# Performance work log

Measured on AMD Instinct MI355X. Metric: run time of the kernel, lower is better.

## Reference

```python
import jax, jax.numpy as jnp
import numpy as np
from jax import lax

B, L, C, H, W = 16, 8, 64, 50, 50
OC, K, PAD = 64, 3, 1
CQ = C // 16


def conv2d(x, w, b, pad):
    y = lax.conv_general_dilated(x, w, (1, 1), [(pad, pad), (pad, pad)],
                                 dimension_numbers=('NCHW', 'OIHW', 'NCHW'))
    return y + b[None, :, None, None]


def attention(x, y, q_w, q_b, k_w, k_b, v_w, v_b):
    # x, y: [b, C, 5, 5]
    b, c, h, w = x.shape
    q = conv2d(x, q_w, q_b, 1).reshape(b, -1, h * w)   # [b, CQ, N]
    kk = conv2d(y, k_w, k_b, 1).reshape(b, -1, h * w)  # [b, CQ, N]
    attn = jax.nn.softmax(jnp.einsum('bcn,bcm->bnm', q, kk), axis=-1)  # [b, Nq, Nk]
    v = conv2d(y, v_w, v_b, 1).reshape(b, c, h * w)    # [b, C, N]
    out = jnp.einsum('bcm,bnm->bcn', v, attn)          # bmm(V, attn^T)
    return out.reshape(b, c, h, w)


def setup_inputs():
    key = jax.random.key(0)
    ks = jax.random.split(key, 15)
    s = 0.05
    return {
        'x': jax.random.normal(ks[0], (B, L, C, H, W), jnp.float32),
        'weight': jax.random.normal(ks[1], (OC, C, K, K), jnp.float32) * s,
        'bias': jax.random.normal(ks[2], (OC,), jnp.float32) * s,
        'init_w': jax.random.normal(ks[3], (C, C, 3, 3), jnp.float32) * s,
        'init_b': jax.random.normal(ks[4], (C,), jnp.float32) * s,
        'q_w': jax.random.normal(ks[5], (CQ, C, 3, 3), jnp.float32) * s,
        'q_b': jax.random.normal(ks[6], (CQ,), jnp.float32) * s,
        'k_w': jax.random.normal(ks[7], (CQ, C, 3, 3), jnp.float32) * s,
        'k_b': jax.random.normal(ks[8], (CQ,), jnp.float32) * s,
        'v_w': jax.random.normal(ks[9], (C, C, 3, 3), jnp.float32) * s,
        'v_b': jax.random.normal(ks[10], (C,), jnp.float32) * s,
        'tconv_w': jax.random.normal(ks[11], (C, C), jnp.float32) * s,  # 1x1x1 Conv3d C->C
        'tconv_b': jax.random.normal(ks[12], (C,), jnp.float32) * s,
        'fc_w': jax.random.normal(ks[13], (C,), jnp.float32) * s,       # 1x1x1 Conv3d C->1
        'fc_b': jax.random.normal(ks[14], (), jnp.float32) * s,
    }


def reference(x, weight, bias, init_w, init_b, q_w, q_b, k_w, k_b, v_w, v_b,
              tconv_w, tconv_b, fc_w, fc_b):
    b, l, c, h, w = x.shape
    # --- generateweight ---
    xet = jnp.transpose(x, (0, 2, 1, 3, 4))  # [b, c, l, h, w]
    # AdaptiveMaxPool3d((None,5,5)); h,w multiples of 5 -> exact reshape max
    pooled = xet.reshape(b, c, l, 5, h // 5, 5, w // 5).max((4, 6))  # [b,c,l,5,5]
    seq = jnp.moveaxis(pooled, 2, 0)  # [l, b, c, 5, 5]
    prior0 = conv2d(seq[0], init_w, init_b, 1)

    def step(prior, xt):
        new = attention(prior, xt, q_w, q_b, k_w, k_b, v_w, v_b)
        return new, new

    _, allp = lax.scan(step, prior0, seq)            # [l, b, c, 5, 5]
    avg = jnp.moveaxis(allp, 0, 2).mean((3, 4))      # AdaptiveAvgPool3d -> [b, c, l]
    calib = jnp.einsum('oc,bcl->bol', tconv_w, avg) + tconv_b[None, :, None]  # [b,c,l]
    scale = 1.0 + jnp.transpose(calib, (0, 2, 1))    # [b, l, c]
    # finalweight[b,l,o,i,kh,kw] = weight[o,i,kh,kw] * scale[b,l,i]
    fw = weight[None, None] * scale[:, :, None, :, None, None]
    fc_out = jnp.einsum('c,bcl->bl', fc_w, avg) + fc_b  # [b, l]
    fb = bias[None, None, :] * (1.0 + fc_out)[:, :, None]  # [b, l, oc]
    # --- grouped conv with groups = b*l ---
    xg = x.reshape(1, b * l * c, h, w)
    wg = fw.reshape(b * l * OC, c, K, K)
    out = lax.conv_general_dilated(xg, wg, (1, 1), [(PAD, PAD), (PAD, PAD)],
                                   feature_group_count=b * l,
                                   dimension_numbers=('NCHW', 'OIHW', 'NCHW'))
    out = out.reshape(b * l, OC, out.shape[-2], out.shape[-1])
    out = out + fb.reshape(b * l, OC)[:, :, None, None]
    return out
```

## Files before the change

kernel.cpp:

```cpp
#include <hip/hip_runtime.h>

typedef short s16x8 __attribute__((ext_vector_type(8)));
typedef float f32x4 __attribute__((ext_vector_type(4)));

__device__ __forceinline__ unsigned short bf16r(float f) {
  unsigned int u = __float_as_uint(f);
  u += 0x7fffu + ((u >> 16) & 1u);
  return (unsigned short)(u >> 16);
}


__global__ __launch_bounds__(256) void poolprep2_kernel(
    const float* __restrict__ x, float* __restrict__ pooled,
    unsigned short* __restrict__ xs) {
  const int blk = blockIdx.x;
  const int g = blk / 10;
  const int rem = blk % 10;
  const int band = rem >> 1;
  const int chalf = rem & 1;
  const int ch0 = chalf * 4;
  const float* xg = x + (size_t)g * 160000;
  unsigned short* xsg = xs + (size_t)g * (52 * 52 * 64);
  __shared__ float pm2[32 * 250];
  const int tid = threadIdx.x;

  for (int task = tid; task < 1000; task += 256) {
    int chunk4 = task & 3;
    int rest = task >> 2;
    int xpair = rest % 25;
    int r = rest / 25;
    int y = band * 10 + r;
    int chunk = ch0 + chunk4;
    const float* base = xg + (chunk * 8) * 2500 + y * 50 + xpair * 2;
    float2 v[8];
#pragma unroll
    for (int k = 0; k < 8; ++k) v[k] = *(const float2*)(base + k * 2500);
#pragma unroll
    for (int k = 0; k < 8; ++k)
      pm2[(chunk4 * 8 + k) * 250 + r * 25 + xpair] = fmaxf(v[k].x, v[k].y);
    uint4 a, b;
    a.x = (unsigned)bf16r(v[0].x) | ((unsigned)bf16r(v[1].x) << 16);
    a.y = (unsigned)bf16r(v[2].x) | ((unsigned)bf16r(v[3].x) << 16);
    a.z = (unsigned)bf16r(v[4].x) | ((unsigned)bf16r(v[5].x) << 16);
    a.w = (unsigned)bf16r(v[6].x) | ((unsigned)bf16r(v[7].x) << 16);
    b.x = (unsigned)bf16r(v[0].y) | ((unsigned)bf16r(v[1].y) << 16);
    b.y = (unsigned)bf16r(v[2].y) | ((unsigned)bf16r(v[3].y) << 16);
    b.z = (unsigned)bf16r(v[4].y) | ((unsigned)bf16r(v[5].y) << 16);
    b.w = (unsigned)bf16r(v[6].y) | ((unsigned)bf16r(v[7].y) << 16);
    int xx = xpair * 2;
    *(uint4*)&xsg[(((y + 1) * 52) + (xx + 1)) * 64 + chunk * 8] = a;
    *(uint4*)&xsg[(((y + 1) * 52) + (xx + 2)) * 64 + chunk * 8] = b;
  }
  uint4 z4;
  z4.x = 0; z4.y = 0; z4.z = 0; z4.w = 0;
  for (int task = tid; task < 80; task += 256) {
    int chunk4 = task & 3;
    int rest = task >> 2;
    int col = (rest & 1) ? 51 : 0;
    int r = rest >> 1;
    int y = band * 10 + r;
    *(uint4*)&xsg[(((y + 1) * 52) + col) * 64 + (ch0 + chunk4) * 8] = z4;
  }
  if (band == 0) {
    for (int task = tid; task < 208; task += 256)
      *(uint4*)&xsg[(task >> 2) * 64 + (ch0 + (task & 3)) * 8] = z4;
  }
  if (band == 4) {
    for (int task = tid; task < 208; task += 256)
      *(uint4*)&xsg[(51 * 52 + (task >> 2)) * 64 + (ch0 + (task & 3)) * 8] = z4;
  }
  __syncthreads();
  if (tid < 160) {
    int c_local = tid / 5, ox = tid % 5;
    const float* pr = &pm2[c_local * 250 + ox * 5];
    float m = -1e30f;
#pragma unroll
    for (int r = 0; r < 10; ++r) {
#pragma unroll
      for (int xp = 0; xp < 5; ++xp) m = fmaxf(m, pr[r * 25 + xp]);
    }
    int c_g = chalf * 32 + c_local;
    pooled[(size_t)g * 1600 + c_g * 25 + band * 5 + ox] = m;
  }
}

__device__ __forceinline__ void conv_pass(
    const unsigned short* in_s, const unsigned short* __restrict__ wg,
    f32x4 acc[4][4], int ikk, int wave, int lane, int l15, int l4) {
#pragma unroll
  for (int dy = 0; dy < 3; ++dy) {
    const int rr = wave + dy;
#pragma unroll
    for (int dx = 0; dx < 3; ++dx) {
      const int tap = dy * 3 + dx;
      s16x8 a[4], bfr[4];
#pragma unroll
      for (int mf = 0; mf < 4; ++mf)
        a[mf] = *reinterpret_cast<const s16x8*>(
            wg + ((((tap * 2 + ikk) * 4 + mf) * 64 + lane) << 3));
#pragma unroll
      for (int nf = 0; nf < 4; ++nf) {
        int cc = nf * 16 + l15 + dx;
        int slot = l4 ^ ((cc ^ (cc >> 2)) & 3);
        bfr[nf] = *reinterpret_cast<const s16x8*>(
            &in_s[((rr * 66 + cc) << 5) + (slot << 3)]);
      }
#pragma unroll
      for (int mf = 0; mf < 4; ++mf)
#pragma unroll
        for (int nf = 0; nf < 4; ++nf)
          acc[mf][nf] = __builtin_amdgcn_mfma_f32_16x16x32_bf16(
              a[mf], bfr[nf], acc[mf][nf], 0, 0, 0);
    }
  }
}

__global__ __launch_bounds__(256, 4) void conv_main_fast2(
    const unsigned short* __restrict__ xs, const unsigned short* __restrict__ wt3,
    const float* __restrict__ fb_g, float* __restrict__ out) {
  const int g = blockIdx.x & 127;
  const int band = blockIdx.x >> 7;
  const int y0 = band * 4;
  const int tid = threadIdx.x;
  __shared__ __align__(16) unsigned short in_s[6 * 66 * 32];
  __shared__ float fb_s[64];
  if (tid < 64) fb_s[tid] = fb_g[g * 64 + tid];

  const unsigned short* xsg = xs + (size_t)g * (52 * 52 * 64);
  const unsigned short* wg = wt3 + (size_t)g * 36864;
  const int wave = tid >> 6, lane = tid & 63;
  const int l15 = lane & 15, l4 = lane >> 4;
  const int yrow = y0 + wave;

  f32x4 acc[4][4];
  f32x4 z = {0.f, 0.f, 0.f, 0.f};
#pragma unroll
  for (int mf = 0; mf < 4; ++mf)
#pragma unroll
    for (int nf = 0; nf < 4; ++nf) acc[mf][nf] = z;

  for (int task = tid; task < 1584; task += 256) {
    int slot = task & 3;
    int c = (task >> 2) % 66;
    int r = (task >> 2) / 66;
    int py = y0 + r;
    int srcSub = slot ^ ((c ^ (c >> 2)) & 3);
    const unsigned short* src = xsg + ((size_t)(py * 52 + c) * 64 + srcSub * 8);
    unsigned short* ldsb = in_s + (size_t)(task & ~63) * 8;
    __builtin_amdgcn_global_load_lds(
        (const __attribute__((address_space(1))) void*)src,
        (__attribute__((address_space(3))) void*)ldsb, 16, 0, 0);
  }
  __syncthreads();
  if (yrow < 50) conv_pass(in_s, wg, acc, 0, wave, lane, l15, l4);
  __syncthreads();
  for (int task = tid; task < 1584; task += 256) {
    int slot = task & 3;
    int c = (task >> 2) % 66;
    int r = (task >> 2) / 66;
    int py = y0 + r;
    int srcSub = slot ^ ((c ^ (c >> 2)) & 3);
    const unsigned short* src = xsg + ((size_t)(py * 52 + c) * 64 + 32 + srcSub * 8);
    unsigned short* ldsb = in_s + (size_t)(task & ~63) * 8;
    __builtin_amdgcn_global_load_lds(
        (const __attribute__((address_space(1))) void*)src,
        (__attribute__((address_space(3))) void*)ldsb, 16, 0, 0);
  }
  __syncthreads();
  if (yrow < 50) {
    conv_pass(in_s, wg, acc, 1, wave, lane, l15, l4);
    float* og = out + (size_t)g * 64 * 2500 + yrow * 50;
#pragma unroll
    for (int mf = 0; mf < 4; ++mf) {
#pragma unroll
      for (int r = 0; r < 4; ++r) {
        int o = mf * 16 + l4 * 4 + r;
        float fbv = fb_s[o];
#pragma unroll
        for (int nf = 0; nf < 4; ++nf) {
          int xx = nf * 16 + l15;
          if (xx < 50) og[(size_t)o * 2500 + xx] = acc[mf][nf][r] + fbv;
        }
      }
    }
  }
}

__global__ __launch_bounds__(256) void calwt_kernel(
    const float* __restrict__ avgg, const float* __restrict__ tconvw,
    const float* __restrict__ tconvb, const float* __restrict__ fcw,
    const float* __restrict__ fcb, const float* __restrict__ bias,
    const float* __restrict__ w, float* __restrict__ fb_g,
    unsigned short* __restrict__ wt3) {
  const int g = blockIdx.x;
  const int tid = threadIdx.x;
  __shared__ float tcw_s[64 * 65];
  __shared__ float av[64];
  __shared__ float sc[64];
  for (int idx = tid; idx < 4096; idx += 256)
    tcw_s[(idx >> 6) * 65 + (idx & 63)] = tconvw[idx];
  if (tid < 64) av[tid] = avgg[g * 64 + tid];
  __syncthreads();
  if (tid < 64) {
    int o = tid;
    float cal = tconvb[o];
#pragma unroll
    for (int c = 0; c < 64; ++c) cal += tcw_s[o * 65 + c] * av[c];
    sc[o] = 1.0f + cal;
    float part = fcw[o] * av[o];
#pragma unroll
    for (int off = 32; off; off >>= 1) part += __shfl_down(part, off);
    float fc = __shfl(part, 0) + fcb[0];
    fb_g[g * 64 + o] = bias[o] * (1.0f + fc);
  }
  __syncthreads();
  unsigned short* outg = wt3 + (size_t)g * 36864;
  for (int idx = tid; idx < 36864; idx += 256) {
    int j = idx & 7;
    int lane = (idx >> 3) & 63;
    int mf = (idx >> 9) & 3;
    int ik = (idx >> 11) & 1;
    int tap = idx >> 12;
    int o = mf * 16 + (lane & 15);
    int i = ik * 32 + 8 * (lane >> 4) + j;
    outg[idx] = bf16r(w[((o * 64) + i) * 9 + tap] * sc[i]);
  }
}


__global__ __launch_bounds__(256) void pool_kernel(const float* __restrict__ x,
                                                   float* __restrict__ pooled) {
  const int blk = blockIdx.x;
  const float* plane = x + (size_t)blk * 2500;
  __shared__ float pmax[250];
  const int t = threadIdx.x;
  if (t < 250) {
    int r = t / 5, cc = t % 5;
    const float* row = plane + r * 50 + cc * 10;
    float m = row[0];
#pragma unroll
    for (int j = 1; j < 10; ++j) m = fmaxf(m, row[j]);
    pmax[r * 5 + cc] = m;
  }
  __syncthreads();
  if (t < 25) {
    int pr = t / 5, cc = t % 5;
    float m = pmax[(pr * 10) * 5 + cc];
#pragma unroll
    for (int rr = 1; rr < 10; ++rr) m = fmaxf(m, pmax[(pr * 10 + rr) * 5 + cc]);
    pooled[(size_t)blk * 25 + t] = m;
  }
}

__global__ __launch_bounds__(256) void wt_kernel(const float* __restrict__ w,
                                                 unsigned short* __restrict__ wt2) {
  int idx = blockIdx.x * 256 + threadIdx.x;
  if (idx >= 36864) return;
  int j = idx & 7;
  int lane = (idx >> 3) & 63;
  int mf = (idx >> 9) & 3;
  int ik = (idx >> 11) & 1;
  int tap = idx >> 12;
  int o = mf * 16 + (lane & 15);
  int i = ik * 32 + 8 * (lane >> 4) + j;
  wt2[idx] = bf16r(w[((o * 64) + i) * 9 + tap]);
}

__global__ __launch_bounds__(256) void conv_main(
    const float* __restrict__ x, const unsigned short* __restrict__ wt2,
    const float* __restrict__ scale_g, const float* __restrict__ fb_g,
    float* __restrict__ out) {
  const int g = blockIdx.x & 127;
  const int band = blockIdx.x >> 7;
  const int y0 = band * 4;
  const int tid = threadIdx.x;
  __shared__ unsigned short in_s[6 * 66 * 64];
  __shared__ float scale_s[64], fb_s[64];
  if (tid < 64) {
    scale_s[tid] = scale_g[g * 64 + tid];
    fb_s[tid] = fb_g[g * 64 + tid];
  }
  __syncthreads();
  const float* xg = x + (size_t)g * 160000;
  for (int task = tid; task < 3168; task += 256) {
    int c = task % 66;
    int rc = task / 66;
    int r = rc >> 3;
    int chunk = rc & 7;
    int y = y0 - 1 + r;
    int xi = c - 1;
    unsigned int p0 = 0, p1 = 0, p2 = 0, p3 = 0;
    if (y >= 0 && y < 50 && xi >= 0 && xi < 50) {
      const float* px = xg + chunk * 8 * 2500 + y * 50 + xi;
      float f0 = px[0] * scale_s[chunk * 8 + 0];
      float f1 = px[2500] * scale_s[chunk * 8 + 1];
      float f2 = px[5000] * scale_s[chunk * 8 + 2];
      float f3 = px[7500] * scale_s[chunk * 8 + 3];
      float f4 = px[10000] * scale_s[chunk * 8 + 4];
      float f5 = px[12500] * scale_s[chunk * 8 + 5];
      float f6 = px[15000] * scale_s[chunk * 8 + 6];
      float f7 = px[17500] * scale_s[chunk * 8 + 7];
      p0 = (unsigned)bf16r(f0) | ((unsigned)bf16r(f1) << 16);
      p1 = (unsigned)bf16r(f2) | ((unsigned)bf16r(f3) << 16);
      p2 = (unsigned)bf16r(f4) | ((unsigned)bf16r(f5) << 16);
      p3 = (unsigned)bf16r(f6) | ((unsigned)bf16r(f7) << 16);
    }
    int chS = chunk ^ (c & 7);
    uint4* dst = (uint4*)&in_s[((r * 66 + c) << 6) + (chS << 3)];
    uint4 u4;
    u4.x = p0; u4.y = p1; u4.z = p2; u4.w = p3;
    *dst = u4;
  }
  __syncthreads();
  const int wave = tid >> 6, lane = tid & 63;
  const int l15 = lane & 15, l4 = lane >> 4;
  const int yrow = y0 + wave;
  if (yrow < 50) {
    f32x4 acc[4][4];
    f32x4 z = {0.f, 0.f, 0.f, 0.f};
#pragma unroll
    for (int mf = 0; mf < 4; ++mf)
#pragma unroll
      for (int nf = 0; nf < 4; ++nf) acc[mf][nf] = z;
#pragma unroll
    for (int dy = 0; dy < 3; ++dy) {
      const int rr = wave + dy;
#pragma unroll
      for (int dx = 0; dx < 3; ++dx) {
        const int tap = dy * 3 + dx;
#pragma unroll
        for (int ik = 0; ik < 2; ++ik) {
          s16x8 a[4], bfr[4];
#pragma unroll
          for (int mf = 0; mf < 4; ++mf)
            a[mf] = *reinterpret_cast<const s16x8*>(
                wt2 + ((((tap * 2 + ik) * 4 + mf) * 64 + lane) << 3));
#pragma unroll
          for (int nf = 0; nf < 4; ++nf) {
            int cc = nf * 16 + l15 + dx;
            int chS = (ik * 4 + l4) ^ (cc & 7);
            bfr[nf] = *reinterpret_cast<const s16x8*>(
                &in_s[((rr * 66 + cc) << 6) + (chS << 3)]);
          }
#pragma unroll
          for (int mf = 0; mf < 4; ++mf)
#pragma unroll
            for (int nf = 0; nf < 4; ++nf)
              acc[mf][nf] = __builtin_amdgcn_mfma_f32_16x16x32_bf16(
                  a[mf], bfr[nf], acc[mf][nf], 0, 0, 0);
        }
      }
    }
    float* og = out + (size_t)g * 64 * 2500 + yrow * 50;
#pragma unroll
    for (int mf = 0; mf < 4; ++mf) {
#pragma unroll
      for (int r = 0; r < 4; ++r) {
        int o = mf * 16 + l4 * 4 + r;
        float fbv = fb_s[o];
#pragma unroll
        for (int nf = 0; nf < 4; ++nf) {
          int xx = nf * 16 + l15;
          if (xx < 50) og[(size_t)o * 2500 + xx] = acc[mf][nf][r] + fbv;
        }
      }
    }
  }
}

__global__ __launch_bounds__(256) void calib_kernel(
    const float* __restrict__ avgg, const float* __restrict__ tconvw,
    const float* __restrict__ tconvb, const float* __restrict__ fcw,
    const float* __restrict__ fcb, const float* __restrict__ bias,
    float* __restrict__ scale_g, float* __restrict__ fb_g) {
  const int tid = threadIdx.x;
  const int wave = tid >> 6, o = tid & 63;
  const int bl = blockIdx.x * 4 + wave;
  __shared__ float tcw_s[64 * 65];
  __shared__ float avgl[4][64];
  for (int idx = tid; idx < 4096; idx += 256)
    tcw_s[(idx >> 6) * 65 + (idx & 63)] = tconvw[idx];
  avgl[wave][o] = avgg[bl * 64 + o];
  __syncthreads();
  float cal = tconvb[o];
  const float* av = avgl[wave];
#pragma unroll
  for (int c = 0; c < 64; ++c) cal += tcw_s[o * 65 + c] * av[c];
  scale_g[bl * 64 + o] = 1.0f + cal;
  float part = fcw[o] * av[o];
#pragma unroll
  for (int off = 32; off; off >>= 1) part += __shfl_down(part, off);
  float fc = __shfl(part, 0) + fcb[0];
  fb_g[bl * 64 + o] = bias[o] * (1.0f + fc);
}


__device__ __forceinline__ void conv64(const float* pool_s, const float* __restrict__ wgt,
                                       const float* __restrict__ bias, float* red,
                                       float* __restrict__ outg, int tid) {
  int co = tid & 63, qd = tid >> 6;
  float acc[25];
#pragma unroll
  for (int n = 0; n < 25; ++n) acc[n] = 0.f;
  for (int ci = qd * 16; ci < qd * 16 + 16; ++ci) {
    float in[25];
#pragma unroll
    for (int n = 0; n < 25; ++n) in[n] = pool_s[ci * 25 + n];
    float w9[9];
#pragma unroll
    for (int tp = 0; tp < 9; ++tp) w9[tp] = wgt[(co * 64 + ci) * 9 + tp];
#pragma unroll
    for (int n = 0; n < 25; ++n) {
      int y = n / 5, xx = n % 5;
#pragma unroll
      for (int dy = 0; dy < 3; ++dy) {
        int yy = y + dy - 1;
        if (yy < 0 || yy > 4) continue;
#pragma unroll
        for (int dx = 0; dx < 3; ++dx) {
          int xc = xx + dx - 1;
          if (xc < 0 || xc > 4) continue;
          acc[n] += in[yy * 5 + xc] * w9[dy * 3 + dx];
        }
      }
    }
  }
#pragma unroll
  for (int n = 0; n < 25; ++n) red[(qd * 64 + co) * 25 + n] = acc[n];
  __syncthreads();
  for (int idx = tid; idx < 1600; idx += 256) {
    float s = red[idx] + red[1600 + idx] + red[3200 + idx] + red[4800 + idx];
    outg[idx] = s + bias[idx / 25];
  }
  __syncthreads();
}

__device__ __forceinline__ void conv4(const float* pool_s, const float* __restrict__ wgt,
                                      const float* __restrict__ bias, float* red,
                                      float* __restrict__ outg, int tid) {
  int co = tid & 3, ci = tid >> 2;
  float acc[25];
#pragma unroll
  for (int n = 0; n < 25; ++n) acc[n] = 0.f;
  float in[25];
#pragma unroll
  for (int n = 0; n < 25; ++n) in[n] = pool_s[ci * 25 + n];
  float w9[9];
#pragma unroll
  for (int tp = 0; tp < 9; ++tp) w9[tp] = wgt[(co * 64 + ci) * 9 + tp];
#pragma unroll
  for (int n = 0; n < 25; ++n) {
    int y = n / 5, xx = n % 5;
#pragma unroll
    for (int dy = 0; dy < 3; ++dy) {
      int yy = y + dy - 1;
      if (yy < 0 || yy > 4) continue;
#pragma unroll
      for (int dx = 0; dx < 3; ++dx) {
        int xc = xx + dx - 1;
        if (xc < 0 || xc > 4) continue;
        acc[n] += in[yy * 5 + xc] * w9[dy * 3 + dx];
      }
    }
  }
#pragma unroll
  for (int n = 0; n < 25; ++n) red[(ci * 4 + co) * 25 + n] = acc[n];
  __syncthreads();
  if (tid < 100) {
    int co2 = tid / 25, n = tid % 25;
    float s = 0.f;
    for (int c = 0; c < 64; ++c) s += red[(c * 4 + co2) * 25 + n];
    outg[co2 * 25 + n] = s + bias[co2];
  }
  __syncthreads();
}

__global__ __launch_bounds__(256) void convB_kernel(
    const float* __restrict__ pooled, const float* __restrict__ vw,
    const float* __restrict__ vb, const float* __restrict__ kw,
    const float* __restrict__ kb, const float* __restrict__ iw,
    const float* __restrict__ ib, float* __restrict__ vconv,
    float* __restrict__ kconv, float* __restrict__ prior0) {
  const int blk = blockIdx.x;
  __shared__ float pool_s[1600];
  __shared__ float red[6400];
  const int tid = threadIdx.x;
  for (int idx = tid; idx < 1600; idx += 256) pool_s[idx] = pooled[blk * 1600 + idx];
  __syncthreads();
  conv64(pool_s, vw, vb, red, vconv + blk * 1600, tid);
  conv4(pool_s, kw, kb, red, kconv + blk * 100, tid);
  if ((blk & 7) == 0) conv64(pool_s, iw, ib, red, prior0 + (blk >> 3) * 1600, tid);
}

__global__ __launch_bounds__(256) void scan2_kernel(
    const float* __restrict__ vconv, const float* __restrict__ kconv,
    const float* __restrict__ prior0, const float* __restrict__ qw,
    const float* __restrict__ qb, float* __restrict__ avgg) {
  const int b = blockIdx.x;
  const int tid = threadIdx.x;
  __shared__ float v_all[8 * 64 * 28];
  __shared__ float kk_all[8 * 100];
  __shared__ float p_s[1600];
  __shared__ float q_s[100];
  __shared__ float qb_s[4];
  __shared__ float attn_s[25 * 28];
  __shared__ float red[100 * 68];
  __shared__ float avgp[64 * 4];
  __shared__ float qw_s[2304];

  for (int idx = tid; idx < 8 * 64 * 28; idx += 256) {
    int m = idx % 28;
    int rest = idx / 28;
    v_all[idx] = (m < 25) ? vconv[b * 12800 + rest * 25 + m] : 0.f;
  }
  for (int idx = tid; idx < 800; idx += 256) kk_all[idx] = kconv[b * 800 + idx];
  for (int idx = tid; idx < 1600; idx += 256) p_s[idx] = prior0[b * 1600 + idx];
  for (int idx = tid; idx < 2304; idx += 256) qw_s[idx] = qw[idx];
  if (tid < 4) qb_s[tid] = qb[tid];
  __syncthreads();

  const int qco = tid & 3, qci = tid >> 2;
  float qwr[9];
#pragma unroll
  for (int tp = 0; tp < 9; ++tp) qwr[tp] = qw_s[(qco * 64 + qci) * 9 + tp];

  for (int l = 0; l < 8; ++l) {
    {
      float in[25];
#pragma unroll
      for (int n = 0; n < 25; ++n) in[n] = p_s[qci * 25 + n];
      float acc[25];
#pragma unroll
      for (int n = 0; n < 25; ++n) acc[n] = 0.f;
#pragma unroll
      for (int n = 0; n < 25; ++n) {
        int y = n / 5, xx = n % 5;
#pragma unroll
        for (int dy = 0; dy < 3; ++dy) {
          int yy = y + dy - 1;
          if (yy < 0 || yy > 4) continue;
#pragma unroll
          for (int dx = 0; dx < 3; ++dx) {
            int xc = xx + dx - 1;
            if (xc < 0 || xc > 4) continue;
            acc[n] += in[yy * 5 + xc] * qwr[dy * 3 + dx];
          }
        }
      }
#pragma unroll
      for (int n = 0; n < 25; ++n) red[(qco * 25 + n) * 68 + qci] = acc[n];
    }
    if (l > 0 && tid < 64) {
      float4 a4 = *(float4*)&avgp[tid * 4];
      avgg[(b * 8 + l - 1) * 64 + tid] = (a4.x + a4.y + a4.z + a4.w) * 0.04f;
    }
    __syncthreads();

    if (tid < 200) {
      int row = tid >> 1, h = tid & 1;
      const float* rp = &red[row * 68 + h * 32];
      float s = 0.f;
#pragma unroll
      for (int j = 0; j < 8; ++j) {
        float4 r4 = *(const float4*)(rp + 4 * j);
        s += r4.x + r4.y + r4.z + r4.w;
      }
      s += __shfl_down(s, 1);
      if (h == 0) q_s[row] = s + qb_s[row / 25];
    }
    __syncthreads();

    if (tid < 25) {
      const int n = tid;
      const float* kk = &kk_all[l * 100];
      float q0 = q_s[n], q1 = q_s[25 + n], q2 = q_s[50 + n], q3 = q_s[75 + n];
      float row[25];
      float mx = -1e30f;
#pragma unroll
      for (int m = 0; m < 25; ++m) {
        float s = q0 * kk[m] + q1 * kk[25 + m] + q2 * kk[50 + m] + q3 * kk[75 + m];
        row[m] = s;
        mx = fmaxf(mx, s);
      }
      float sm = 0.f;
#pragma unroll
      for (int m = 0; m < 25; ++m) {
        float e = __expf(row[m] - mx);
        row[m] = e;
        sm += e;
      }
      float inv = 1.0f / sm;
#pragma unroll
      for (int m = 0; m < 25; ++m) attn_s[n * 28 + m] = row[m] * inv;
      attn_s[n * 28 + 25] = 0.f;
      attn_s[n * 28 + 26] = 0.f;
      attn_s[n * 28 + 27] = 0.f;
    }
    __syncthreads();

    {
      const int c = tid & 63, grp = tid >> 6;
      float4 v4[7];
      const float* vr = &v_all[(l * 64 + c) * 28];
#pragma unroll
      for (int j = 0; j < 7; ++j) v4[j] = *(const float4*)(vr + 4 * j);
      float partial = 0.f;
      for (int n = grp; n < 25; n += 4) {
        const float* ar = &attn_s[n * 28];
        float acc = 0.f;
#pragma unroll
        for (int j = 0; j < 7; ++j) {
          float4 a4 = *(const float4*)(ar + 4 * j);
          acc += v4[j].x * a4.x + v4[j].y * a4.y + v4[j].z * a4.z + v4[j].w * a4.w;
        }
        p_s[c * 25 + n] = acc;
        partial += acc;
      }
      avgp[c * 4 + grp] = partial;
    }
    __syncthreads();
  }
  if (tid < 64) {
    float4 a4 = *(float4*)&avgp[tid * 4];
    avgg[(b * 8 + 7) * 64 + tid] = (a4.x + a4.y + a4.z + a4.w) * 0.04f;
  }
}

extern "C" void kernel_launch(void* const* d_in, const int* in_sizes, int n_in,
                              void* d_out, int out_size, void* d_ws, size_t ws_size,
                              hipStream_t stream) {
  const float* x       = (const float*)d_in[0];
  const float* weight  = (const float*)d_in[1];
  const float* bias    = (const float*)d_in[2];
  const float* init_w  = (const float*)d_in[3];
  const float* init_b  = (const float*)d_in[4];
  const float* q_w     = (const float*)d_in[5];
  const float* q_b     = (const float*)d_in[6];
  const float* k_w     = (const float*)d_in[7];
  const float* k_b     = (const float*)d_in[8];
  const float* v_w     = (const float*)d_in[9];
  const float* v_b     = (const float*)d_in[10];
  const float* tconv_w = (const float*)d_in[11];
  const float* tconv_b = (const float*)d_in[12];
  const float* fc_w    = (const float*)d_in[13];
  const float* fc_b    = (const float*)d_in[14];
  float* out = (float*)d_out;

  float* ws = (float*)d_ws;
  float* pooled = ws;
  float* vconv  = ws + 204800;
  float* kconv  = ws + 409600;
  float* prior0 = ws + 422400;
  float* scaleg = ws + 448000;
  float* fbg    = ws + 456192;
  float* avgg   = ws + 464384;
  unsigned short* wt3 = (unsigned short*)(ws + 472576);
  unsigned short* xsb = wt3 + 4718592;

  const size_t NEED_FAST = 55695360ull;

  if (ws_size >= NEED_FAST) {
    poolprep2_kernel<<<1280, 256, 0, stream>>>(x, pooled, xsb);
    convB_kernel<<<128, 256, 0, stream>>>(pooled, v_w, v_b, k_w, k_b, init_w, init_b,
                                          vconv, kconv, prior0);
    scan2_kernel<<<16, 256, 0, stream>>>(vconv, kconv, prior0, q_w, q_b, avgg);
    calwt_kernel<<<128, 256, 0, stream>>>(avgg, tconv_w, tconv_b, fc_w, fc_b, bias,
                                          weight, fbg, wt3);
    conv_main_fast2<<<13 * 128, 256, 0, stream>>>(xsb, wt3, fbg, out);
  } else {
    unsigned short* wt2 = (unsigned short*)(ws + 472576);
    pool_kernel<<<8192, 256, 0, stream>>>(x, pooled);
    wt_kernel<<<144, 256, 0, stream>>>(weight, wt2);
    convB_kernel<<<128, 256, 0, stream>>>(pooled, v_w, v_b, k_w, k_b, init_w, init_b,
                                          vconv, kconv, prior0);
    scan2_kernel<<<16, 256, 0, stream>>>(vconv, kconv, prior0, q_w, q_b, avgg);
    calib_kernel<<<32, 256, 0, stream>>>(avgg, tconv_w, tconv_b, fc_w, fc_b, bias,
                                         scaleg, fbg);
    conv_main<<<13 * 128, 256, 0, stream>>>(x, wt2, scaleg, fbg, out);
  }
}
```

Before: 163.0 us.

## Store V in padded bf16 layout and vectorize scan loads; simplify LDS swizzle

The conv producer now writes V as bf16 rows padded to 40, K interleaved as float4 per position, and prior padded to 28, so the scan kernel can stage everything with 16-byte copies instead of scalar strided gathers. Attention weights and V are held in bf16 in LDS, which halves LDS traffic in the serial scan. The LDS swizzle in the main conv is simplified to (c>>1)&3. Rounding V and attn to bf16 adds precision loss in the calibration path, and the new swizzle may change bank conflict behaviour.

```diff
diff --git a/kernel.cpp b/kernel.cpp
--- a/kernel.cpp
+++ b/kernel.cpp
@@ -2,11 +2,18 @@
 
 typedef short s16x8 __attribute__((ext_vector_type(8)));
 typedef float f32x4 __attribute__((ext_vector_type(4)));
+typedef unsigned int u32x4 __attribute__((ext_vector_type(4)));
 
 __device__ __forceinline__ unsigned short bf16r(float f) {
   unsigned int u = __float_as_uint(f);
   u += 0x7fffu + ((u >> 16) & 1u);
   return (unsigned short)(u >> 16);
+}
+__device__ __forceinline__ float bf_lo(unsigned int u) {
+  return __uint_as_float(u << 16);
+}
+__device__ __forceinline__ float bf_hi(unsigned int u) {
+  return __uint_as_float(u & 0xffff0000u);
 }
 
 
@@ -101,7 +108,7 @@
 #pragma unroll
       for (int nf = 0; nf < 4; ++nf) {
         int cc = nf * 16 + l15 + dx;
-        int slot = l4 ^ ((cc ^ (cc >> 2)) & 3);
+        int slot = l4 ^ ((cc >> 1) & 3);
         bfr[nf] = *reinterpret_cast<const s16x8*>(
             &in_s[((rr * 66 + cc) << 5) + (slot << 3)]);
       }
@@ -144,7 +151,7 @@
     int c = (task >> 2) % 66;
     int r = (task >> 2) / 66;
     int py = y0 + r;
-    int srcSub = slot ^ ((c ^ (c >> 2)) & 3);
+    int srcSub = slot ^ ((c >> 1) & 3);
     const unsigned short* src = xsg + ((size_t)(py * 52 + c) * 64 + srcSub * 8);
     unsigned short* ldsb = in_s + (size_t)(task & ~63) * 8;
     __builtin_amdgcn_global_load_lds(
@@ -159,7 +166,7 @@
     int c = (task >> 2) % 66;
     int r = (task >> 2) / 66;
     int py = y0 + r;
-    int srcSub = slot ^ ((c ^ (c >> 2)) & 3);
+    int srcSub = slot ^ ((c >> 1) & 3);
     const unsigned short* src = xsg + ((size_t)(py * 52 + c) * 64 + 32 + srcSub * 8);
     unsigned short* ldsb = in_s + (size_t)(task & ~63) * 8;
     __builtin_amdgcn_global_load_lds(
@@ -224,6 +231,279 @@
     int o = mf * 16 + (lane & 15);
     int i = ik * 32 + 8 * (lane >> 4) + j;
     outg[idx] = bf16r(w[((o * 64) + i) * 9 + tap] * sc[i]);
+  }
+}
+
+
+__device__ __forceinline__ void conv64core(const float* pool_s,
+                                           const float* __restrict__ wgt,
+                                           float* red, int tid) {
+  int co = tid & 63, qd = tid >> 6;
+  float acc[25];
+#pragma unroll
+  for (int n = 0; n < 25; ++n) acc[n] = 0.f;
+  for (int ci = qd * 16; ci < qd * 16 + 16; ++ci) {
+    float in[25];
+#pragma unroll
+    for (int n = 0; n < 25; ++n) in[n] = pool_s[ci * 25 + n];
+    float w9[9];
+#pragma unroll
+    for (int tp = 0; tp < 9; ++tp) w9[tp] = wgt[(co * 64 + ci) * 9 + tp];
+#pragma unroll
+    for (int n = 0; n < 25; ++n) {
+      int y = n / 5, xx = n % 5;
+#pragma unroll
+      for (int dy = 0; dy < 3; ++dy) {
+        int yy = y + dy - 1;
+        if (yy < 0 || yy > 4) continue;
+#pragma unroll
+        for (int dx = 0; dx < 3; ++dx) {
+          int xc = xx + dx - 1;
+          if (xc < 0 || xc > 4) continue;
+          acc[n] += in[yy * 5 + xc] * w9[dy * 3 + dx];
+        }
+      }
+    }
+  }
+#pragma unroll
+  for (int n = 0; n < 25; ++n) red[(qd * 64 + co) * 25 + n] = acc[n];
+  __syncthreads();
+}
+
+__global__ __launch_bounds__(256) void convB2_kernel(
+    const float* __restrict__ pooled, const float* __restrict__ vw,
+    const float* __restrict__ vb, const float* __restrict__ kw,
+    const float* __restrict__ kb, const float* __restrict__ iw,
+    const float* __restrict__ ib, unsigned short* __restrict__ vbg,
+    float* __restrict__ kk4g, float* __restrict__ p28g) {
+  const int blk = blockIdx.x;
+  __shared__ float pool_s[1600];
+  __shared__ float red[6400];
+  const int tid = threadIdx.x;
+  for (int idx = tid; idx < 1600; idx += 256) pool_s[idx] = pooled[blk * 1600 + idx];
+  __syncthreads();
+
+  conv64core(pool_s, vw, red, tid);
+  {
+    unsigned short* dst = vbg + (size_t)blk * 2560;
+    for (int idx = tid; idx < 1600; idx += 256) {
+      float s = red[idx] + red[1600 + idx] + red[3200 + idx] + red[4800 + idx];
+      dst[(idx / 25) * 40 + idx % 25] = bf16r(s + vb[idx / 25]);
+    }
+    for (int idx = tid; idx < 960; idx += 256)
+      dst[(idx / 15) * 40 + 25 + idx % 15] = 0;
+  }
+  __syncthreads();
+
+  {
+    int co = tid & 3, ci = tid >> 2;
+    float acc[25];
+#pragma unroll
+    for (int n = 0; n < 25; ++n) acc[n] = 0.f;
+    float in[25];
+#pragma unroll
+    for (int n = 0; n < 25; ++n) in[n] = pool_s[ci * 25 + n];
+    float w9[9];
+#pragma unroll
+    for (int tp = 0; tp < 9; ++tp) w9[tp] = kw[(co * 64 + ci) * 9 + tp];
+#pragma unroll
+    for (int n = 0; n < 25; ++n) {
+      int y = n / 5, xx = n % 5;
+#pragma unroll
+      for (int dy = 0; dy < 3; ++dy) {
+        int yy = y + dy - 1;
+        if (yy < 0 || yy > 4) continue;
+#pragma unroll
+        for (int dx = 0; dx < 3; ++dx) {
+          int xc = xx + dx - 1;
+          if (xc < 0 || xc > 4) continue;
+          acc[n] += in[yy * 5 + xc] * w9[dy * 3 + dx];
+        }
+      }
+    }
+#pragma unroll
+    for (int n = 0; n < 25; ++n) red[(ci * 4 + co) * 25 + n] = acc[n];
+  }
+  __syncthreads();
+  if (tid < 100) {
+    int co = tid / 25, m = tid % 25;
+    float s = 0.f;
+    for (int c = 0; c < 64; ++c) s += red[(c * 4 + co) * 25 + m];
+    kk4g[blk * 100 + m * 4 + co] = s + kb[co];
+  }
+  __syncthreads();
+
+  if ((blk & 7) == 0) {
+    conv64core(pool_s, iw, red, tid);
+    float* dst = p28g + (size_t)(blk >> 3) * 1792;
+    for (int idx = tid; idx < 1600; idx += 256) {
+      float s = red[idx] + red[1600 + idx] + red[3200 + idx] + red[4800 + idx];
+      dst[(idx / 25) * 28 + idx % 25] = s + ib[idx / 25];
+    }
+  }
+}
+
+
+__global__ __launch_bounds__(256) void scan3_kernel(
+    const unsigned short* __restrict__ vbg, const float* __restrict__ kk4g,
+    const float* __restrict__ p28g, const float* __restrict__ qw,
+    const float* __restrict__ qb, float* __restrict__ avgg) {
+  const int b = blockIdx.x;
+  const int tid = threadIdx.x;
+  __shared__ __align__(16) unsigned short v_bf[8 * 64 * 40];
+  __shared__ __align__(16) unsigned short attn_bf[25 * 32];
+  __shared__ float p_s[64 * 28];
+  __shared__ float red[100 * 68];
+  __shared__ f32x4 kk4_s[8 * 25];
+  __shared__ float q_s[100];
+  __shared__ float qw_s[2304];
+  __shared__ float avgp[256];
+  __shared__ float qb_s[4];
+
+  {
+    const u32x4* vs = (const u32x4*)(vbg + (size_t)b * 20480);
+    u32x4* vd = (u32x4*)v_bf;
+    for (int i = tid; i < 2560; i += 256) vd[i] = vs[i];
+    const f32x4* ks = (const f32x4*)(kk4g + b * 800);
+    for (int i = tid; i < 200; i += 256) kk4_s[i] = ks[i];
+    const f32x4* ps = (const f32x4*)(p28g + (size_t)b * 1792);
+    f32x4* pd = (f32x4*)p_s;
+    for (int i = tid; i < 448; i += 256) pd[i] = ps[i];
+    const f32x4* qs = (const f32x4*)qw;
+    f32x4* qd = (f32x4*)qw_s;
+    for (int i = tid; i < 576; i += 256) qd[i] = qs[i];
+    if (tid < 4) qb_s[tid] = qb[tid];
+  }
+  __syncthreads();
+
+  const int qco = tid & 3, qci = tid >> 2;
+  float qwr[9];
+#pragma unroll
+  for (int tp = 0; tp < 9; ++tp) qwr[tp] = qw_s[(qco * 64 + qci) * 9 + tp];
+
+#pragma unroll 1
+  for (int l = 0; l < 8; ++l) {
+    {
+      f32x4 i4[7];
+      const f32x4* pr = (const f32x4*)&p_s[qci * 28];
+#pragma unroll
+      for (int j = 0; j < 7; ++j) i4[j] = pr[j];
+      float in[25];
+#pragma unroll
+      for (int n = 0; n < 25; ++n) in[n] = i4[n >> 2][n & 3];
+      float acc[25];
+#pragma unroll
+      for (int n = 0; n < 25; ++n) acc[n] = 0.f;
+#pragma unroll
+      for (int n = 0; n < 25; ++n) {
+        int y = n / 5, xx = n % 5;
+#pragma unroll
+        for (int dy = 0; dy < 3; ++dy) {
+          int yy = y + dy - 1;
+          if (yy < 0 || yy > 4) continue;
+#pragma unroll
+          for (int dx = 0; dx < 3; ++dx) {
+            int xc = xx + dx - 1;
+            if (xc < 0 || xc > 4) continue;
+            acc[n] += in[yy * 5 + xc] * qwr[dy * 3 + dx];
+          }
+        }
+      }
+#pragma unroll
+      for (int n = 0; n < 25; ++n) red[(qco * 25 + n) * 68 + qci] = acc[n];
+    }
+    if (l > 0 && tid < 64) {
+      f32x4 a4 = *(const f32x4*)&avgp[tid * 4];
+      avgg[(b * 8 + l - 1) * 64 + tid] = (a4[0] + a4[1] + a4[2] + a4[3]) * 0.04f;
+    }
+    __syncthreads();
+
+    if (tid < 200) {
+      int row = tid >> 1, h = tid & 1;
+      const f32x4* rp = (const f32x4*)&red[row * 68 + h * 32];
+      float s = 0.f;
+#pragma unroll
+      for (int j = 0; j < 8; ++j) {
+        f32x4 r4 = rp[j];
+        s += r4[0] + r4[1] + r4[2] + r4[3];
+      }
+      s += __shfl_down(s, 1);
+      if (h == 0) q_s[row] = s + qb_s[row / 25];
+    }
+    __syncthreads();
+
+    if (tid < 25) {
+      const int n = tid;
+      const f32x4* kk = &kk4_s[l * 25];
+      float q0 = q_s[n], q1 = q_s[25 + n], q2 = q_s[50 + n], q3 = q_s[75 + n];
+      float row[25];
+      float mx = -1e30f;
+#pragma unroll
+      for (int m = 0; m < 25; ++m) {
+        f32x4 k4 = kk[m];
+        float s = q0 * k4[0] + q1 * k4[1] + q2 * k4[2] + q3 * k4[3];
+        row[m] = s;
+        mx = fmaxf(mx, s);
+      }
+      float sm = 0.f;
+#pragma unroll
+      for (int m = 0; m < 25; ++m) {
+        float e = __expf(row[m] - mx);
+        row[m] = e;
+        sm += e;
+      }
+      float inv = 1.0f / sm;
+      unsigned int w16[16];
+#pragma unroll
+      for (int j = 0; j < 16; ++j) {
+        float lo = (2 * j < 25) ? row[2 * j] * inv : 0.f;
+        float hi = (2 * j + 1 < 25) ? row[2 * j + 1] * inv : 0.f;
+        w16[j] = (unsigned)bf16r(lo) | ((unsigned)bf16r(hi) << 16);
+      }
+      u32x4* ad = (u32x4*)&attn_bf[n * 32];
+      u32x4 d0 = {w16[0], w16[1], w16[2], w16[3]};
+      u32x4 d1 = {w16[4], w16[5], w16[6], w16[7]};
+      u32x4 d2 = {w16[8], w16[9], w16[10], w16[11]};
+      u32x4 d3 = {w16[12], w16[13], w16[14], w16[15]};
+      ad[0] = d0; ad[1] = d1; ad[2] = d2; ad[3] = d3;
+    }
+    __syncthreads();
+
+    {
+      const int c = tid & 63, grp = tid >> 6;
+      const u32x4* vr = (const u32x4*)&v_bf[(l * 64 + c) * 40];
+      u32x4 vv[4];
+#pragma unroll
+      for (int j = 0; j < 4; ++j) vv[j] = vr[j];
+      float vf[25];
+#pragma unroll
+      for (int m = 0; m < 25; ++m) {
+        unsigned int u = vv[m >> 3][(m >> 1) & 3];
+        vf[m] = (m & 1) ? bf_hi(u) : bf_lo(u);
+      }
+      float partial = 0.f;
+      for (int n = grp; n < 25; n += 4) {
+        const u32x4* ar = (const u32x4*)&attn_bf[n * 32];
+        u32x4 aa[4];
+#pragma unroll
+        for (int j = 0; j < 4; ++j) aa[j] = ar[j];
+        float acc = 0.f;
+#pragma unroll
+        for (int m = 0; m < 25; ++m) {
+          unsigned int u = aa[m >> 3][(m >> 1) & 3];
+          float a = (m & 1) ? bf_hi(u) : bf_lo(u);
+          acc += vf[m] * a;
+        }
+        p_s[c * 28 + n] = acc;
+        partial += acc;
+      }
+      avgp[(c << 2) + grp] = partial;
+    }
+    __syncthreads();
+  }
+  if (tid < 64) {
+    f32x4 a4 = *(const f32x4*)&avgp[tid * 4];
+    avgg[(b * 8 + 7) * 64 + tid] = (a4[0] + a4[1] + a4[2] + a4[3]) * 0.04f;
   }
 }
 
@@ -394,238 +674,6 @@
   fb_g[bl * 64 + o] = bias[o] * (1.0f + fc);
 }
 
-
-__device__ __forceinline__ void conv64(const float* pool_s, const float* __restrict__ wgt,
-                                       const float* __restrict__ bias, float* red,
-                                       float* __restrict__ outg, int tid) {
-  int co = tid & 63, qd = tid >> 6;
-  float acc[25];
-#pragma unroll
-  for (int n = 0; n < 25; ++n) acc[n] = 0.f;
-  for (int ci = qd * 16; ci < qd * 16 + 16; ++ci) {
-    float in[25];
-#pragma unroll
-    for (int n = 0; n < 25; ++n) in[n] = pool_s[ci * 25 + n];
-    float w9[9];
-#pragma unroll
-    for (int tp = 0; tp < 9; ++tp) w9[tp] = wgt[(co * 64 + ci) * 9 + tp];
-#pragma unroll
-    for (int n = 0; n < 25; ++n) {
-      int y = n / 5, xx = n % 5;
-#pragma unroll
-      for (int dy = 0; dy < 3; ++dy) {
-        int yy = y + dy - 1;
-        if (yy < 0 || yy > 4) continue;
-#pragma unroll
-        for (int dx = 0; dx < 3; ++dx) {
-          int xc = xx + dx - 1;
-          if (xc < 0 || xc > 4) continue;
-          acc[n] += in[yy * 5 + xc] * w9[dy * 3 + dx];
-        }
-      }
-    }
-  }
-#pragma unroll
-  for (int n = 0; n < 25; ++n) red[(qd * 64 + co) * 25 + n] = acc[n];
-  __syncthreads();
-  for (int idx = tid; idx < 1600; idx += 256) {
-    float s = red[idx] + red[1600 + idx] + red[3200 + idx] + red[4800 + idx];
-    outg[idx] = s + bias[idx / 25];
-  }
-  __syncthreads();
-}
-
-__device__ __forceinline__ void conv4(const float* pool_s, const float* __restrict__ wgt,
-                                      const float* __restrict__ bias, float* red,
-                                      float* __restrict__ outg, int tid) {
-  int co = tid & 3, ci = tid >> 2;
-  float acc[25];
-#pragma unroll
-  for (int n = 0; n < 25; ++n) acc[n] = 0.f;
-  float in[25];
-#pragma unroll
-  for (int n = 0; n < 25; ++n) in[n] = pool_s[ci * 25 + n];
-  float w9[9];
-#pragma unroll
-  for (int tp = 0; tp < 9; ++tp) w9[tp] = wgt[(co * 64 + ci) * 9 + tp];
-#pragma unroll
-  for (int n = 0; n < 25; ++n) {
-    int y = n / 5, xx = n % 5;
-#pragma unroll
-    for (int dy = 0; dy < 3; ++dy) {
-      int yy = y + dy - 1;
-      if (yy < 0 || yy > 4) continue;
-#pragma unroll
-      for (int dx = 0; dx < 3; ++dx) {
-        int xc = xx + dx - 1;
-        if (xc < 0 || xc > 4) continue;
-        acc[n] += in[yy * 5 + xc] * w9[dy * 3 + dx];
-      }
-    }
-  }
-#pragma unroll
-  for (int n = 0; n < 25; ++n) red[(ci * 4 + co) * 25 + n] = acc[n];
-  __syncthreads();
-  if (tid < 100) {
-    int co2 = tid / 25, n = tid % 25;
-    float s = 0.f;
-    for (int c = 0; c < 64; ++c) s += red[(c * 4 + co2) * 25 + n];
-    outg[co2 * 25 + n] = s + bias[co2];
-  }
-  __syncthreads();
-}
-
-__global__ __launch_bounds__(256) void convB_kernel(
-    const float* __restrict__ pooled, const float* __restrict__ vw,
-    const float* __restrict__ vb, const float* __restrict__ kw,
-    const float* __restrict__ kb, const float* __restrict__ iw,
-    const float* __restrict__ ib, float* __restrict__ vconv,
-    float* __restrict__ kconv, float* __restrict__ prior0) {
-  const int blk = blockIdx.x;
-  __shared__ float pool_s[1600];
-  __shared__ float red[6400];
-  const int tid = threadIdx.x;
-  for (int idx = tid; idx < 1600; idx += 256) pool_s[idx] = pooled[blk * 1600 + idx];
-  __syncthreads();
-  conv64(pool_s, vw, vb, red, vconv + blk * 1600, tid);
-  conv4(pool_s, kw, kb, red, kconv + blk * 100, tid);
-  if ((blk & 7) == 0) conv64(pool_s, iw, ib, red, prior0 + (blk >> 3) * 1600, tid);
-}
-
-__global__ __launch_bounds__(256) void scan2_kernel(
-    const float* __restrict__ vconv, const float* __restrict__ kconv,
-    const float* __restrict__ prior0, const float* __restrict__ qw,
-    const float* __restrict__ qb, float* __restrict__ avgg) {
-  const int b = blockIdx.x;
-  const int tid = threadIdx.x;
-  __shared__ float v_all[8 * 64 * 28];
-  __shared__ float kk_all[8 * 100];
-  __shared__ float p_s[1600];
-  __shared__ float q_s[100];
-  __shared__ float qb_s[4];
-  __shared__ float attn_s[25 * 28];
-  __shared__ float red[100 * 68];
-  __shared__ float avgp[64 * 4];
-  __shared__ float qw_s[2304];
-
-  for (int idx = tid; idx < 8 * 64 * 28; idx += 256) {
-    int m = idx % 28;
-    int rest = idx / 28;
-    v_all[idx] = (m < 25) ? vconv[b * 12800 + rest * 25 + m] : 0.f;
-  }
-  for (int idx = tid; idx < 800; idx += 256) kk_all[idx] = kconv[b * 800 + idx];
-  for (int idx = tid; idx < 1600; idx += 256) p_s[idx] = prior0[b * 1600 + idx];
-  for (int idx = tid; idx < 2304; idx += 256) qw_s[idx] = qw[idx];
-  if (tid < 4) qb_s[tid] = qb[tid];
-  __syncthreads();
-
-  const int qco = tid & 3, qci = tid >> 2;
-  float qwr[9];
-#pragma unroll
-  for (int tp = 0; tp < 9; ++tp) qwr[tp] = qw_s[(qco * 64 + qci) * 9 + tp];
-
-  for (int l = 0; l < 8; ++l) {
-    {
-      float in[25];
-#pragma unroll
-      for (int n = 0; n < 25; ++n) in[n] = p_s[qci * 25 + n];
-      float acc[25];
-#pragma unroll
-      for (int n = 0; n < 25; ++n) acc[n] = 0.f;
-#pragma unroll
-      for (int n = 0; n < 25; ++n) {
-        int y = n / 5, xx = n % 5;
-#pragma unroll
-        for (int dy = 0; dy < 3; ++dy) {
-          int yy = y + dy - 1;
-          if (yy < 0 || yy > 4) continue;
-#pragma unroll
-          for (int dx = 0; dx < 3; ++dx) {
-            int xc = xx + dx - 1;
-            if (xc < 0 || xc > 4) continue;
-            acc[n] += in[yy * 5 + xc] * qwr[dy * 3 + dx];
-          }
-        }
-      }
-#pragma unroll
-      for (int n = 0; n < 25; ++n) red[(qco * 25 + n) * 68 + qci] = acc[n];
-    }
-    if (l > 0 && tid < 64) {
-      float4 a4 = *(float4*)&avgp[tid * 4];
-      avgg[(b * 8 + l - 1) * 64 + tid] = (a4.x + a4.y + a4.z + a4.w) * 0.04f;
-    }
-    __syncthreads();
-
-    if (tid < 200) {
-      int row = tid >> 1, h = tid & 1;
-      const float* rp = &red[row * 68 + h * 32];
-      float s = 0.f;
-#pragma unroll
-      for (int j = 0; j < 8; ++j) {
-        float4 r4 = *(const float4*)(rp + 4 * j);
-        s += r4.x + r4.y + r4.z + r4.w;
-      }
-      s += __shfl_down(s, 1);
-      if (h == 0) q_s[row] = s + qb_s[row / 25];
-    }
-    __syncthreads();
-
-    if (tid < 25) {
-      const int n = tid;
-      const float* kk = &kk_all[l * 100];
-      float q0 = q_s[n], q1 = q_s[25 + n], q2 = q_s[50 + n], q3 = q_s[75 + n];
-      float row[25];
-      float mx = -1e30f;
-#pragma unroll
-      for (int m = 0; m < 25; ++m) {
-        float s = q0 * kk[m] + q1 * kk[25 + m] + q2 * kk[50 + m] + q3 * kk[75 + m];
-        row[m] = s;
-        mx = fmaxf(mx, s);
-      }
-      float sm = 0.f;
-#pragma unroll
-      for (int m = 0; m < 25; ++m) {
-        float e = __expf(row[m] - mx);
-        row[m] = e;
-        sm += e;
-      }
-      float inv = 1.0f / sm;
-#pragma unroll
-      for (int m = 0; m < 25; ++m) attn_s[n * 28 + m] = row[m] * inv;
-      attn_s[n * 28 + 25] = 0.f;
-      attn_s[n * 28 + 26] = 0.f;
-      attn_s[n * 28 + 27] = 0.f;
-    }
-    __syncthreads();
-
-    {
-      const int c = tid & 63, grp = tid >> 6;
-      float4 v4[7];
-      const float* vr = &v_all[(l * 64 + c) * 28];
-#pragma unroll
-      for (int j = 0; j < 7; ++j) v4[j] = *(const float4*)(vr + 4 * j);
-      float partial = 0.f;
-      for (int n = grp; n < 25; n += 4) {
-        const float* ar = &attn_s[n * 28];
-        float acc = 0.f;
-#pragma unroll
-        for (int j = 0; j < 7; ++j) {
-          float4 a4 = *(const float4*)(ar + 4 * j);
-          acc += v4[j].x * a4.x + v4[j].y * a4.y + v4[j].z * a4.z + v4[j].w * a4.w;
-        }
-        p_s[c * 25 + n] = acc;
-        partial += acc;
-      }
-      avgp[c * 4 + grp] = partial;
-    }
-    __syncthreads();
-  }
-  if (tid < 64) {
-    float4 a4 = *(float4*)&avgp[tid * 4];
-    avgg[(b * 8 + 7) * 64 + tid] = (a4.x + a4.y + a4.z + a4.w) * 0.04f;
-  }
-}
-
 extern "C" void kernel_launch(void* const* d_in, const int* in_sizes, int n_in,
                               void* d_out, int out_size, void* d_ws, size_t ws_size,
                               hipStream_t stream) {
@@ -648,32 +696,32 @@
 
   float* ws = (float*)d_ws;
   float* pooled = ws;
-  float* vconv  = ws + 204800;
-  float* kconv  = ws + 409600;
-  float* prior0 = ws + 422400;
-  float* scaleg = ws + 448000;
-  float* fbg    = ws + 456192;
-  float* avgg   = ws + 464384;
-  unsigned short* wt3 = (unsigned short*)(ws + 472576);
+  unsigned short* vbg = (unsigned short*)(ws + 204800);
+  float* kk4g   = ws + 368640;
+  float* p28g   = ws + 381440;
+  float* scaleg = ws + 410112;
+  float* fbg    = ws + 418304;
+  float* avgg   = ws + 426496;
+  unsigned short* wt3 = (unsigned short*)(ws + 434688);
   unsigned short* xsb = wt3 + 4718592;
 
-  const size_t NEED_FAST = 55695360ull;
+  const size_t NEED_FAST = 55543808ull;
 
   if (ws_size >= NEED_FAST) {
     poolprep2_kernel<<<1280, 256, 0, stream>>>(x, pooled, xsb);
-    convB_kernel<<<128, 256, 0, stream>>>(pooled, v_w, v_b, k_w, k_b, init_w, init_b,
-                                          vconv, kconv, prior0);
-    scan2_kernel<<<16, 256, 0, stream>>>(vconv, kconv, prior0, q_w, q_b, avgg);
+    convB2_kernel<<<128, 256, 0, stream>>>(pooled, v_w, v_b, k_w, k_b, init_w,
+                                           init_b, vbg, kk4g, p28g);
+    scan3_kernel<<<16, 256, 0, stream>>>(vbg, kk4g, p28g, q_w, q_b, avgg);
     calwt_kernel<<<128, 256, 0, stream>>>(avgg, tconv_w, tconv_b, fc_w, fc_b, bias,
                                           weight, fbg, wt3);
     conv_main_fast2<<<13 * 128, 256, 0, stream>>>(xsb, wt3, fbg, out);
   } else {
-    unsigned short* wt2 = (unsigned short*)(ws + 472576);
+    unsigned short* wt2 = (unsigned short*)(ws + 434688);
     pool_kernel<<<8192, 256, 0, stream>>>(x, pooled);
     wt_kernel<<<144, 256, 0, stream>>>(weight, wt2);
-    convB_kernel<<<128, 256, 0, stream>>>(pooled, v_w, v_b, k_w, k_b, init_w, init_b,
-                                          vconv, kconv, prior0);
-    scan2_kernel<<<16, 256, 0, stream>>>(vconv, kconv, prior0, q_w, q_b, avgg);
+    convB2_kernel<<<128, 256, 0, stream>>>(pooled, v_w, v_b, k_w, k_b, init_w,
+                                           init_b, vbg, kk4g, p28g);
+    scan3_kernel<<<16, 256, 0, stream>>>(vbg, kk4g, p28g, q_w, q_b, avgg);
     calib_kernel<<<32, 256, 0, stream>>>(avgg, tconv_w, tconv_b, fc_w, fc_b, bias,
                                          scaleg, fbg);
     conv_main<<<13 * 128, 256, 0, stream>>>(x, wt2, scaleg, fbg, out);
```

New measurement: 149.7 us. 1.09x faster.
